# Kernel tuning notes

Hardware: AMD Instinct MI355X
Metric: run time of the kernel (lower is better)

Reference implementation:

```python
import jax, jax.numpy as jnp
import numpy as np


def setup_inputs() -> dict:
    key = jax.random.key(0)
    ks = jax.random.split(key, 5)
    B, IN, OUT = 8192, 4096, 4096
    in_q, out_q = IN // 4, OUT // 4
    # xavier-uniform-like scale for weights
    lim = float(np.sqrt(6.0 / (in_q + out_q)))
    return {
        "x": jax.random.normal(ks[0], (B, IN), dtype=jnp.float32),
        "Wa": jax.random.uniform(ks[1], (in_q, out_q), jnp.float32, -lim, lim),
        "Wb": jax.random.uniform(ks[2], (in_q, out_q), jnp.float32, -lim, lim),
        "Wc": jax.random.uniform(ks[3], (in_q, out_q), jnp.float32, -lim, lim),
        "Wd": jax.random.uniform(ks[4], (in_q, out_q), jnp.float32, -lim, lim),
        "bias": jnp.zeros((OUT,), dtype=jnp.float32),
    }


def reference(x, Wa, Wb, Wc, Wd, bias):
    # split quaternion components: [B, in_q] each
    a, b, c, d = jnp.split(x, 4, axis=1)
    # Hamilton product with weight quaternion (right multiplication)
    out_a = a @ Wa - b @ Wb - c @ Wc - d @ Wd
    out_b = a @ Wb + b @ Wa + c @ Wd - d @ Wc
    out_c = a @ Wc - b @ Wd + c @ Wa + d @ Wb
    out_d = a @ Wd + b @ Wc - c @ Wb + d @ Wa
    return jnp.concatenate([out_a, out_b, out_c, out_d], axis=1) + bias
```

## Files before the change

kernel.cpp:

```cpp
#include <hip/hip_runtime.h>
#include <hip/hip_bf16.h>
#include <cstdint>
#include <cstddef>

typedef __bf16 bf16_t;
typedef __bf16 bf16x4 __attribute__((ext_vector_type(4)));
typedef __bf16 bf16x8 __attribute__((ext_vector_type(8)));
typedef float f32x4 __attribute__((ext_vector_type(4)));

#define GLD16(src, dst)                                                       \
    __builtin_amdgcn_global_load_lds(                                         \
        (const __attribute__((address_space(1))) void*)(src),                 \
        (__attribute__((address_space(3))) void*)(dst), 16, 0, 0)

#define BAR() asm volatile("s_barrier" ::: "memory")
#define WAIT_VM4() asm volatile("s_waitcnt vmcnt(4)" ::: "memory")
#define WAIT_VM6() asm volatile("s_waitcnt vmcnt(6)" ::: "memory")
#define WAIT_VM0() asm volatile("s_waitcnt vmcnt(0)" ::: "memory")

__global__ __launch_bounds__(256) void cvt_x_kernel(const float* __restrict__ x,
                                                    bf16_t* __restrict__ xb, int n4) {
    int idx = blockIdx.x * blockDim.x + threadIdx.x;
    int stride = gridDim.x * blockDim.x;
    const f32x4* xv = (const f32x4*)x;
    bf16x4* ov = (bf16x4*)xb;
    for (int i = idx; i < n4; i += stride) {
        f32x4 v = xv[i];
        bf16x4 o;
        o[0] = (bf16_t)v[0];
        o[1] = (bf16_t)v[1];
        o[2] = (bf16_t)v[2];
        o[3] = (bf16_t)v[3];
        ov[i] = o;
    }
}

__global__ __launch_bounds__(256) void pack_w_kernel(const float* __restrict__ Wa,
                                                     const float* __restrict__ Wb,
                                                     const float* __restrict__ Wc,
                                                     const float* __restrict__ Wd,
                                                     bf16_t* __restrict__ Mt) {
    __shared__ float tile[64][65];
    const int kb = blockIdx.x * 64;
    const int nb = blockIdx.y * 64;
    const int i = kb >> 10;
    const int j = nb >> 10;

    const float* W[4] = {Wa, Wb, Wc, Wd};
    const int srcIdx[4][4] = {{0, 1, 2, 3}, {1, 0, 3, 2}, {2, 3, 0, 1}, {3, 2, 1, 0}};
    const float sgn[4][4] = {{1.f, 1.f, 1.f, 1.f},
                             {-1.f, 1.f, -1.f, 1.f},
                             {-1.f, 1.f, 1.f, -1.f},
                             {-1.f, -1.f, 1.f, 1.f}};
    const float* Ws = W[srcIdx[i][j]];
    const float s = sgn[i][j];

    const int kq = kb & 1023;
    const int nq = nb & 1023;
    const int tx = threadIdx.x & 63;
    const int ty = threadIdx.x >> 6;

    for (int r = ty; r < 64; r += 4)
        tile[r][tx] = Ws[(size_t)(kq + r) * 1024 + (nq + tx)];
    __syncthreads();
    for (int r = ty; r < 64; r += 4)
        Mt[(size_t)(nb + r) * 4096 + (kb + tx)] = (bf16_t)(s * tile[tx][r]);
}

__global__ __launch_bounds__(512, 2) void qgemm_kernel(const bf16_t* __restrict__ A,
                                                       const bf16_t* __restrict__ Bt,
                                                       const float* __restrict__ bias,
                                                       float* __restrict__ C) {
    constexpr int N = 4096, K = 4096;
    constexpr int NT = K / 64;
    extern __shared__ __align__(16) char lds[];

    const int tid = threadIdx.x;
    const int w = tid >> 6;
    const int lane = tid & 63;
    const int l15 = lane & 15, l4 = lane >> 4;
    const int wr = w >> 2, wc = w & 3;

    const int wg = blockIdx.x;
    const int swz = (wg & 7) * 64 + (wg >> 3);
    const int brow = (swz >> 4) * 256;
    const int bcol = (swz & 15) * 256;

    const int srow = lane >> 3;
    const int skb = (lane & 7) ^ (lane >> 3);

    auto stageA = [&](int buf, int h, int tt) {
#pragma unroll
        for (int q = 0; q < 2; ++q) {
            const bf16_t* src = A + (size_t)(brow + h * 128 + w * 16 + q * 8 + srow) * K +
                                tt * 64 + skb * 8;
            GLD16(src, lds + buf * 32768 + h * 16384 + w * 2048 + q * 1024);
        }
    };
    auto stageB = [&](int buf, int h, int tt) {
#pragma unroll
        for (int q = 0; q < 2; ++q) {
            const bf16_t* src = Bt + (size_t)(bcol + h * 128 + w * 16 + q * 8 + srow) * K +
                                tt * 64 + skb * 8;
            GLD16(src, lds + 65536 + buf * 32768 + h * 16384 + w * 2048 + q * 1024);
        }
    };

    f32x4 acc[8][4] = {};
    bf16x8 a[4][2], b0[2][2], b1[2][2];

    auto ldAm = [&](int buf, int mh, int m) {
#pragma unroll
        for (int c = 0; c < 2; ++c)
            a[m][c] = *(const bf16x8*)(lds + buf * 32768 + wr * 16384 +
                                       (mh * 64 + m * 16 + l15) * 128 +
                                       ((c * 4 + l4) ^ (l15 & 7)) * 16);
    };
    auto ldB = [&](int buf, int nh, bf16x8(&b)[2][2]) {
#pragma unroll
        for (int n = 0; n < 2; ++n)
#pragma unroll
            for (int c = 0; c < 2; ++c)
                b[n][c] = *(const bf16x8*)(lds + 65536 + buf * 32768 + nh * 16384 +
                                           (wc * 32 + n * 16 + l15) * 128 +
                                           ((c * 4 + l4) ^ (l15 & 7)) * 16);
    };
    auto mmac = [&](int mh, int nh, bf16x8(&b)[2][2]) {
        __builtin_amdgcn_s_setprio(1);
#pragma unroll
        for (int c = 0; c < 2; ++c)
#pragma unroll
            for (int m = 0; m < 4; ++m)
#pragma unroll
                for (int n = 0; n < 2; ++n)
                    acc[mh * 4 + m][nh * 2 + n] = __builtin_amdgcn_mfma_f32_16x16x32_bf16(
                        a[m][c], b[n][c], acc[mh * 4 + m][nh * 2 + n], 0, 0, 0);
        __builtin_amdgcn_s_setprio(0);
    };

#define TILE_BODY(CUR, TT)                                                    \
    {                                                                         \
        const int tt = (TT);                                                  \
                             \
        if (tt + 1 < NT) stageA((CUR) ^ 1, 1, tt + 1);                        \
        BAR();                                                                \
        ldAm((CUR), 0, 2);                                                    \
        ldAm((CUR), 0, 3);                                                    \
        mmac(0, 0, b0);                                                       \
        ldB((CUR), 1, b1);                                                    \
        BAR();                                                                \
                             \
        if (tt + 2 < NT) stageB((CUR), 0, tt + 2);                            \
        BAR();                                                                \
        mmac(0, 1, b1);                                                       \
        ldAm((CUR), 1, 0);                                                    \
        ldAm((CUR), 1, 1);                                                    \
        BAR();                                                                \
              \
        if (tt + 2 < NT) stageB((CUR), 1, tt + 2);                            \
        BAR();                                                                \
        ldAm((CUR), 1, 2);                                                    \
        ldAm((CUR), 1, 3);                                                    \
        mmac(1, 1, b1);                                                       \
        if (tt + 2 < NT) {                                                    \
            WAIT_VM4();                                                       \
        } else {                                                              \
            WAIT_VM0();                                                       \
        }                                                                     \
        BAR();                                                                \
             \
        if (tt + 2 < NT) stageA((CUR), 0, tt + 2);                            \
        BAR();                                                                \
        mmac(1, 0, b0);                                                       \
        if (tt + 1 < NT) {                                                    \
            ldB((CUR) ^ 1, 0, b0);                                            \
            ldAm((CUR) ^ 1, 0, 0);                                            \
            ldAm((CUR) ^ 1, 0, 1);                                            \
        }                                                                     \
        BAR();                                                                \
    }

    stageA(0, 0, 0);
    stageA(0, 1, 0);
    stageB(0, 0, 0);
    stageB(0, 1, 0);
    stageB(1, 0, 1);
    stageB(1, 1, 1);
    stageA(1, 0, 1);
    WAIT_VM6();
    BAR();
    ldB(0, 0, b0);
    ldAm(0, 0, 0);
    ldAm(0, 0, 1);

    for (int it = 0; it < NT / 2; ++it) {
        TILE_BODY(0, 2 * it);
        TILE_BODY(1, 2 * it + 1);
    }
#undef TILE_BODY

#pragma unroll
    for (int n = 0; n < 4; ++n) {
        const int col = bcol + (n >> 1) * 128 + wc * 32 + (n & 1) * 16 + l15;
        const float bv = bias[col];
#pragma unroll
        for (int m = 0; m < 8; ++m) {
            const int row0 = brow + wr * 128 + m * 16 + l4 * 4;
            const f32x4 v = acc[m][n];
#pragma unroll
            for (int i = 0; i < 4; ++i)
                C[(size_t)(row0 + i) * N + col] = v[i] + bv;
        }
    }
}

extern "C" void kernel_launch(void* const* d_in, const int* in_sizes, int n_in,
                              void* d_out, int out_size, void* d_ws, size_t ws_size,
                              hipStream_t stream) {
    const float* x = (const float*)d_in[0];
    const float* Wa = (const float*)d_in[1];
    const float* Wb = (const float*)d_in[2];
    const float* Wc = (const float*)d_in[3];
    const float* Wd = (const float*)d_in[4];
    const float* bias = (const float*)d_in[5];
    float* out = (float*)d_out;

    const int M = 8192, N = 4096, K = 4096;

    bf16_t* xb = (bf16_t*)d_ws;
    bf16_t* Mt = xb + (size_t)M * K;

    cvt_x_kernel<<<4096, 256, 0, stream>>>(x, xb, (M * K) / 4);
    pack_w_kernel<<<dim3(64, 64), 256, 0, stream>>>(Wa, Wb, Wc, Wd, Mt);

    (void)hipFuncSetAttribute((const void*)qgemm_kernel,
                              hipFuncAttributeMaxDynamicSharedMemorySize, 131072);
    qgemm_kernel<<<dim3((M / 256) * (N / 256)), 512, 131072, stream>>>(xb, Mt, bias, out);
}
```

Measured before the change: 282.3 us.

## Double-buffer A fragments in registers and drop intermediate barriers in GEMM loop

Splits the A-operand register fragments into two full sets (a0/a1) so the whole next half-tile of A is loaded from LDS while MFMAs run on the current one, instead of loading two rows at a time. It also removes roughly half of the s_barrier calls per tile iteration, cutting synchronization stalls between the four waves. The cost is more VGPRs for the second A set, which may lower occupancy or cause spills. Fewer barriers also narrow the margin on LDS buffer reuse ordering.

Result: slower. 451.3 us (+59.9%).

```diff
diff --git a/kernel.cpp b/kernel.cpp
--- a/kernel.cpp
+++ b/kernel.cpp
@@ -107,14 +107,16 @@
     };
 
     f32x4 acc[8][4] = {};
-    bf16x8 a[4][2], b0[2][2], b1[2][2];
-
-    auto ldAm = [&](int buf, int mh, int m) {
-#pragma unroll
-        for (int c = 0; c < 2; ++c)
-            a[m][c] = *(const bf16x8*)(lds + buf * 32768 + wr * 16384 +
-                                       (mh * 64 + m * 16 + l15) * 128 +
-                                       ((c * 4 + l4) ^ (l15 & 7)) * 16);
+    bf16x8 a0[4][2], a1[4][2], b0[2][2], b1[2][2];
+
+    auto ldAset = [&](int buf, int mh, bf16x8(&a)[4][2]) {
+#pragma unroll
+        for (int m = 0; m < 4; ++m)
+#pragma unroll
+            for (int c = 0; c < 2; ++c)
+                a[m][c] = *(const bf16x8*)(lds + buf * 32768 + wr * 16384 +
+                                           (mh * 64 + m * 16 + l15) * 128 +
+                                           ((c * 4 + l4) ^ (l15 & 7)) * 16);
     };
     auto ldB = [&](int buf, int nh, bf16x8(&b)[2][2]) {
 #pragma unroll
@@ -125,7 +127,7 @@
                                            (wc * 32 + n * 16 + l15) * 128 +
                                            ((c * 4 + l4) ^ (l15 & 7)) * 16);
     };
-    auto mmac = [&](int mh, int nh, bf16x8(&b)[2][2]) {
+    auto mmac = [&](bf16x8(&a)[4][2], int mh, int nh, bf16x8(&b)[2][2]) {
         __builtin_amdgcn_s_setprio(1);
 #pragma unroll
         for (int c = 0; c < 2; ++c)
@@ -141,41 +143,31 @@
 #define TILE_BODY(CUR, TT)                                                    \
     {                                                                         \
         const int tt = (TT);                                                  \
-                             \
+            \
         if (tt + 1 < NT) stageA((CUR) ^ 1, 1, tt + 1);                        \
-        BAR();                                                                \
-        ldAm((CUR), 0, 2);                                                    \
-        ldAm((CUR), 0, 3);                                                    \
-        mmac(0, 0, b0);                                                       \
         ldB((CUR), 1, b1);                                                    \
-        BAR();                                                                \
-                             \
+        mmac(a0, 0, 0, b0);                                                   \
+        BAR();                                                                \
+                        \
         if (tt + 2 < NT) stageB((CUR), 0, tt + 2);                            \
-        BAR();                                                                \
-        mmac(0, 1, b1);                                                       \
-        ldAm((CUR), 1, 0);                                                    \
-        ldAm((CUR), 1, 1);                                                    \
-        BAR();                                                                \
-              \
+        ldAset((CUR), 1, a1);                                                 \
+        mmac(a0, 0, 1, b1);                                                   \
+        BAR();                                                                \
+                        \
         if (tt + 2 < NT) stageB((CUR), 1, tt + 2);                            \
-        BAR();                                                                \
-        ldAm((CUR), 1, 2);                                                    \
-        ldAm((CUR), 1, 3);                                                    \
-        mmac(1, 1, b1);                                                       \
+        mmac(a1, 1, 1, b1);                                                   \
         if (tt + 2 < NT) {                                                    \
             WAIT_VM4();                                                       \
         } else {                                                              \
             WAIT_VM0();                                                       \
         }                                                                     \
         BAR();                                                                \
-             \
+              \
         if (tt + 2 < NT) stageA((CUR), 0, tt + 2);                            \
-        BAR();                                                                \
-        mmac(1, 0, b0);                                                       \
+        mmac(a1, 1, 0, b0);                                                   \
         if (tt + 1 < NT) {                                                    \
             ldB((CUR) ^ 1, 0, b0);                                            \
-            ldAm((CUR) ^ 1, 0, 0);                                            \
-            ldAm((CUR) ^ 1, 0, 1);                                            \
+            ldAset((CUR) ^ 1, 0, a0);                                         \
         }                                                                     \
         BAR();                                                                \
     }
@@ -190,8 +182,7 @@
     WAIT_VM6();
     BAR();
     ldB(0, 0, b0);
-    ldAm(0, 0, 0);
-    ldAm(0, 0, 1);
+    ldAset(0, 0, a0);
 
     for (int it = 0; it < NT / 2; ++it) {
         TILE_BODY(0, 2 * it);
```
